# Optimization experiments

Measured on AMD Instinct MI355X. Metric: run time of the kernel, lower is better.

## Reference

```python
import jax, jax.numpy as jnp
import numpy as np

N_HEAD = 16


def _rotate_half(x):
    # interleaved split then concat, exactly as the torch module does
    x1 = x[..., ::2]
    x2 = x[..., 1::2]
    return jnp.concatenate((-x2, x1), axis=-1)


def setup_inputs() -> dict:
    key = jax.random.key(0)
    k1, k2, k3 = jax.random.split(key, 3)
    B, T, C = 4, 2048, 2048
    x = jax.random.normal(k1, (B, T, C), dtype=jnp.float32)
    w_attn = jax.random.normal(k2, (3 * C, C), dtype=jnp.float32) * 0.02
    b_attn = jnp.zeros((3 * C,), dtype=jnp.float32)
    w_proj = jax.random.normal(k3, (C, C), dtype=jnp.float32) * 0.02
    b_proj = jnp.zeros((C,), dtype=jnp.float32)
    return {"x": x, "w_attn": w_attn, "b_attn": b_attn, "w_proj": w_proj, "b_proj": b_proj}


def reference(x, w_attn, b_attn, w_proj, b_proj):
    B, T, C = x.shape
    H = N_HEAD
    D = C // H

    qkv = x @ w_attn.T + b_attn  # (B, T, 3C)
    q, k, v = jnp.split(qkv, 3, axis=2)
    # (B, H, T, D)
    q = q.reshape(B, T, H, D).transpose(0, 2, 1, 3)
    k = k.reshape(B, T, H, D).transpose(0, 2, 1, 3)
    v = v.reshape(B, T, H, D).transpose(0, 2, 1, 3)

    # RoPE tables (buffer inv_freq computed from head_dim)
    inv_freq = 1.0 / (10000.0 ** (jnp.arange(0, D, 2, dtype=jnp.float32) / D))
    t = jnp.arange(T, dtype=jnp.float32)
    freqs = t[:, None] * inv_freq[None, :]            # (T, D/2)
    emb = jnp.concatenate((freqs, freqs), axis=-1)    # (T, D)
    cos, sin = jnp.cos(emb), jnp.sin(emb)

    # module's (nonstandard) rotary application: returns q_cos + q_sin
    rq, rk = _rotate_half(q), _rotate_half(k)
    q = (q * cos - rq * sin) + (q * sin + rq * cos)
    k = (k * cos - rk * sin) + (k * sin + rk * cos)

    # causal SDPA
    scale = 1.0 / jnp.sqrt(jnp.asarray(D, dtype=x.dtype))
    scores = jnp.einsum("bhqd,bhkd->bhqk", q, k) * scale
    causal = jnp.tril(jnp.ones((T, T), dtype=bool))
    scores = jnp.where(causal, scores, jnp.asarray(-1e30, dtype=scores.dtype))
    att = jax.nn.softmax(scores, axis=-1)
    y = jnp.einsum("bhqk,bhkd->bhqd", att, v)

    y = y.transpose(0, 2, 1, 3).reshape(B, T, C)
    return y @ w_proj.T + b_proj
```

## Files before the change

### kernel.cpp

```cpp
#include <hip/hip_runtime.h>

#define T_SEQ 2048
#define DHEAD 128
#define NHEAD 16
#define CDIM  2048
#define BATCH 4

typedef __bf16 v8bf __attribute__((ext_vector_type(8)));
typedef __bf16 v4bf __attribute__((ext_vector_type(4)));
typedef __bf16 v2bf __attribute__((ext_vector_type(2)));
typedef float  v4f  __attribute__((ext_vector_type(4)));

#define MFMA16(a,b,c) __builtin_amdgcn_mfma_f32_16x16x32_bf16(a,b,c,0,0,0)
#define GLDS16(g,l) __builtin_amdgcn_global_load_lds( \
    (__attribute__((address_space(1))) void*)(g), \
    (__attribute__((address_space(3))) void*)(l), 16, 0, 0)

__global__ __launch_bounds__(256) void cvt_all(const float* __restrict__ x,
                                               const float* __restrict__ wa,
                                               const float* __restrict__ wp,
                                               __bf16* __restrict__ xo,
                                               __bf16* __restrict__ wao,
                                               __bf16* __restrict__ wpo,
                                               float2* __restrict__ rt) {
  int i = blockIdx.x * 256 + threadIdx.x;
  int stride = gridDim.x * 256;
  for (int j = i; j < 8519680; j += stride) {
    if (j < 8388608) {
      const float* src; __bf16* dst; int off;
      if (j < 4194304)      { src = x;  dst = xo;  off = j; }
      else if (j < 7340032) { src = wa; dst = wao; off = j - 4194304; }
      else                  { src = wp; dst = wpo; off = j - 7340032; }
      float4 v = *(const float4*)(src + (size_t)off * 4);
      v4bf o = {(__bf16)v.x, (__bf16)v.y, (__bf16)v.z, (__bf16)v.w};
      *(v4bf*)(dst + (size_t)off * 4) = o;
    } else {
      int e = j - 8388608;
      int tt = e >> 6, jj = e & 63;
      float invf = exp2f((float)jj * (-13.287712379549449f / 64.f));
      float ang = (float)tt * invf;
      float c = cosf(ang), s = sinf(ang);
      rt[e] = make_float2(c + s, c - s);
    }
  }
}

#define LGKM0() { asm volatile("s_waitcnt lgkmcnt(0)" ::: "memory"); \
                  __builtin_amdgcn_sched_barrier(0); }
#define BARR()  { __builtin_amdgcn_s_barrier(); __builtin_amdgcn_sched_barrier(0); }

#define RDA(mm, kk) (*(const v8bf*)(bA + (wm16 + (mm)*32 + lr) * 128 + ((((kk)*64) + lgc) ^ swl)))
#define RDB(n, kk)  (*(const v8bf*)(bB + (wn64 + (n)*16 + lr) * 128 + ((((kk)*64) + lgc) ^ swl)))
#define MF(mm,n,kk) acc[mm][n] = MFMA16(af[(mm)&1][kk], bfr[n][kk], acc[mm][n]);

#define PH_MFMA(MM0, MM1) \
  BARR(); LGKM0(); \
  __builtin_amdgcn_s_setprio(1); \
  MF(MM0,0,0) MF(MM0,1,0) MF(MM0,2,0) MF(MM0,3,0) \
  MF(MM1,0,0) MF(MM1,1,0) MF(MM1,2,0) MF(MM1,3,0) \
  MF(MM0,0,1) MF(MM0,1,1) MF(MM0,2,1) MF(MM0,3,1) \
  MF(MM1,0,1) MF(MM1,1,1) MF(MM1,2,1) MF(MM1,3,1) \
  __builtin_amdgcn_s_setprio(0); \
  BARR();

#define STAGE_H(SRC, ks, hh, LBASE) { \
  GLDS16((SRC) + (size_t)((hh)*128)      * 2048 + (size_t)(ks)*64, lds + (LBASE) + dst0); \
  GLDS16((SRC) + (size_t)((hh)*128 + 64) * 2048 + (size_t)(ks)*64, lds + (LBASE) + 4096 + dst0); }

#define TILE(CB, ks1, ks2) { \
  const char* bA = (const char*)(lds + (CB)*32768); \
  const char* bB = bA + 32768; \
  v8bf bfr[4][2], af[2][2]; \
  af[0][0]=RDA(0,0); af[0][1]=RDA(0,1); af[1][0]=RDA(1,0); af[1][1]=RDA(1,1); \
  bfr[0][0]=RDB(0,0); bfr[0][1]=RDB(0,1); bfr[1][0]=RDB(1,0); bfr[1][1]=RDB(1,1); \
  bfr[2][0]=RDB(2,0); bfr[2][1]=RDB(2,1); bfr[3][0]=RDB(3,0); bfr[3][1]=RDB(3,1); \
  STAGE_H(Asrc, ks1, 1, ((CB)^1)*32768 + 8192); \
  PH_MFMA(0, 1) \
  af[0][0]=RDA(2,0); af[0][1]=RDA(2,1); af[1][0]=RDA(3,0); af[1][1]=RDA(3,1); \
  STAGE_H(Bsrc, ks2, 0, (CB)*32768 + 16384); \
  PH_MFMA(2, 3) \
  af[0][0]=RDA(4,0); af[0][1]=RDA(4,1); af[1][0]=RDA(5,0); af[1][1]=RDA(5,1); \
  STAGE_H(Asrc, ks2, 0, (CB)*32768); \
  PH_MFMA(4, 5) \
  af[0][0]=RDA(6,0); af[0][1]=RDA(6,1); af[1][0]=RDA(7,0); af[1][1]=RDA(7,1); \
  STAGE_H(Bsrc, ks2, 1, (CB)*32768 + 24576); \
  asm volatile("s_waitcnt vmcnt(6)" ::: "memory"); \
  PH_MFMA(6, 7) \
}

__device__ __forceinline__ void gemm256_core(
    const __bf16* __restrict__ A, const __bf16* __restrict__ Bm,
    int row0, int col0, __bf16* lds, v4f (&acc)[8][4],
    int wm16, int wn64, int lr, int lg) {
  int t = threadIdx.x;
  int wid = t >> 6;
  int lgc = lg * 16;
  int swl = (lr & 7) << 4;
#pragma unroll
  for (int mm = 0; mm < 8; ++mm)
#pragma unroll
    for (int n = 0; n < 4; ++n) acc[mm][n] = (v4f){0.f, 0.f, 0.f, 0.f};

  int srow = t >> 3;
  int scol = (((t & 7) ^ ((t >> 3) & 7)) << 3);
  const __bf16* Asrc = A  + (size_t)(row0 + srow) * 2048 + scol;
  const __bf16* Bsrc = Bm + (size_t)(col0 + srow) * 2048 + scol;
  int dst0 = wid << 9;

  STAGE_H(Asrc, 0, 0, 0);
  STAGE_H(Asrc, 0, 1, 8192);
  STAGE_H(Bsrc, 0, 0, 16384);
  STAGE_H(Bsrc, 0, 1, 24576);
  STAGE_H(Bsrc, 1, 0, 32768 + 16384);
  STAGE_H(Asrc, 1, 0, 32768);
  STAGE_H(Bsrc, 1, 1, 32768 + 24576);
  asm volatile("s_waitcnt vmcnt(6)" ::: "memory");
  BARR();

  for (int m = 0; m < 32; m += 2) {
    TILE(0, m + 1, (m + 2) & 31)
    TILE(1, (m + 2) & 31, (m + 3) & 31)
  }
  asm volatile("s_waitcnt vmcnt(0)" ::: "memory");
}

__global__ __launch_bounds__(512, 2) void gemm_qkv8(
    const __bf16* __restrict__ A, const __bf16* __restrict__ Bm,
    const float* __restrict__ bias, const float2* __restrict__ rt,
    __bf16* __restrict__ Qb, __bf16* __restrict__ Kb, __bf16* __restrict__ Vt) {
  extern __shared__ __bf16 lds[];
  int t = threadIdx.x, wid = t >> 6, l = t & 63;
  int lr = l & 15, lg = l >> 4;
  int wm16 = (wid >> 2) * 16, wn64 = (wid & 3) * 64;
  int bid = blockIdx.x;
  int xcd = bid & 7, idx = bid >> 3;
  int res = idx & 31, grp = idx >> 5;
  int row0 = (xcd * 4 + (res >> 3)) * 256;
  int col0 = (grp * 8 + (res & 7)) * 256;
  v4f acc[8][4];
  gemm256_core(A, Bm, row0, col0, lds, acc, wm16, wn64, lr, lg);

  if (col0 >= 4096) {
    int h0 = (col0 & 2047) >> 7;
    int bb = row0 >> 11;
    int t0 = row0 & 2047;
    int d_r = t >> 1, half = t & 1;
    int hh = h0 + (d_r >> 7), dd = d_r & 127;
#pragma unroll
    for (int mm = 0; mm < 8; ++mm) {
      __syncthreads();
#pragma unroll
      for (int n = 0; n < 4; ++n) {
        int d_loc = wn64 + n * 16 + lr;
        float bv = bias[col0 + d_loc];
        v4bf pv = {(__bf16)(acc[mm][n][0] + bv), (__bf16)(acc[mm][n][1] + bv),
                   (__bf16)(acc[mm][n][2] + bv), (__bf16)(acc[mm][n][3] + bv)};
        *(v4bf*)&lds[d_loc * 40 + wm16 + lg * 4] = pv;
      }
      __syncthreads();
      size_t vbase = ((size_t)((bb * NHEAD + hh) * DHEAD + dd)) * T_SEQ
                   + t0 + mm * 32 + half * 16;
      v8bf x0 = *(const v8bf*)&lds[d_r * 40 + half * 16];
      v8bf x1 = *(const v8bf*)&lds[d_r * 40 + half * 16 + 8];
      *(v8bf*)&Vt[vbase] = x0;
      *(v8bf*)&Vt[vbase + 8] = x1;
    }
    return;
  }

  __syncthreads();
#pragma unroll
  for (int n = 0; n < 4; ++n) {
    int c_loc = wn64 + n * 16 + lr;
    float bv = bias[col0 + c_loc];
#pragma unroll
    for (int mm = 0; mm < 8; ++mm) {
#pragma unroll
      for (int rr = 0; rr < 4; ++rr) {
        int r_loc = wm16 + mm * 32 + lg * 4 + rr;
        *(__bf16*)((char*)lds + r_loc * 512 + ((2 * c_loc) ^ ((r_loc & 31) << 4)))
            = (__bf16)(acc[mm][n][rr] + bv);
      }
    }
  }
  __syncthreads();
  {
    int tensor = col0 >> 11;
    int h0 = (col0 & 2047) >> 7;
    int bb = row0 >> 11;
    int t0 = row0 & 2047;
    __bf16* QK = tensor ? Kb : Qb;
    int d = l;
    float sgn = (d < 32) ? -1.f : 1.f;
    int mOff = 4 * d;
    int pOff = (d < 32) ? (8 * d) : (8 * d - 256);
    int tOff = ((2 * d) & 63) * 8;
#pragma unroll 4
    for (int i = 0; i < 64; ++i) {
      int p = wid * 64 + i;
      int u = p >> 8, r = p & 255;
      int tt = t0 + r;
      const char* lrow_ = (const char*)lds + r * 512;
      int swz = (r & 31) << 4;
      int cb = u * 256;
      v2bf xm = *(const v2bf*)(lrow_ + ((cb + mOff) ^ swz));
      v4bf xp = *(const v4bf*)(lrow_ + ((cb + pOff) ^ swz));
      float4 tv = *(const float4*)((const char*)(rt + (size_t)tt * 64) + tOff);
      float p1 = (d < 32) ? (float)xp[1] : (float)xp[0];
      float p2 = (d < 32) ? (float)xp[3] : (float)xp[2];
      float o1 = (float)xm[0] * tv.x + sgn * p1 * tv.y;
      float o2 = (float)xm[1] * tv.z + sgn * p2 * tv.w;
      v2bf ov = {(__bf16)o1, (__bf16)o2};
      __bf16* dst = QK + ((size_t)(bb * NHEAD + h0 + u) * T_SEQ + tt) * DHEAD;
      *(v2bf*)(dst + 2 * d) = ov;
    }
  }
}

__global__ __launch_bounds__(512, 2) void gemm_out8(
    const __bf16* __restrict__ A, const __bf16* __restrict__ Bm,
    const float* __restrict__ bias, float* __restrict__ C) {
  extern __shared__ __bf16 lds[];
  int t = threadIdx.x, wid = t >> 6, l = t & 63;
  int lr = l & 15, lg = l >> 4;
  int wm16 = (wid >> 2) * 16, wn64 = (wid & 3) * 64;
  int bid = blockIdx.x;
  int xcd = bid & 7, idx = bid >> 3;
  int row0 = (xcd * 4 + idx / 8) * 256;
  int col0 = (idx % 8) * 256;
  v4f acc[8][4];
  gemm256_core(A, Bm, row0, col0, lds, acc, wm16, wn64, lr, lg);
#pragma unroll
  for (int n = 0; n < 4; ++n) {
    int col = col0 + wn64 + n * 16 + lr;
    float bv = bias[col];
#pragma unroll
    for (int mm = 0; mm < 8; ++mm) {
#pragma unroll
      for (int rr = 0; rr < 4; ++rr) {
        int mg = row0 + wm16 + mm * 32 + lg * 4 + rr;
        C[(size_t)mg * CDIM + col] = acc[mm][n][rr] + bv;
      }
    }
  }
}

__global__ __launch_bounds__(512, 2) void attn_fwd(
    const __bf16* __restrict__ Qb, const __bf16* __restrict__ Kb,
    const __bf16* __restrict__ Vt, __bf16* __restrict__ Y) {
  __shared__ __bf16 lK[64 * 128];
  __shared__ __bf16 lV[128 * 64];
  __shared__ __bf16 plds[8][16][72];
  int t = threadIdx.x, w = t >> 6, l = t & 63;
  int lr = l & 15, lg = l >> 4;
  int id = blockIdx.x;
  int xcd = id & 7, s = id >> 3;
  int bh = xcd * 8 + (s & 7);
  int g = s >> 3;
  int k = (g < 4) ? (7 - g) : (g - 4);
  int qb = k * 256;
  int b = bh >> 4, h = bh & 15;
  int q0 = qb + w * 32;
  const __bf16* Qh = Qb + (size_t)bh * T_SEQ * DHEAD;
  const __bf16* Kh = Kb + (size_t)bh * T_SEQ * DHEAD;
  const __bf16* Vh = Vt + (size_t)bh * DHEAD * T_SEQ;

  v8bf qf[2][4];
#pragma unroll
  for (int j = 0; j < 2; ++j)
#pragma unroll
    for (int c = 0; c < 4; ++c)
      qf[j][c] = *(const v8bf*)&Qh[(size_t)(q0 + j * 16 + lr) * DHEAD + c * 32 + lg * 8];

  v4f o[2][8];
#pragma unroll
  for (int j = 0; j < 2; ++j)
#pragma unroll
    for (int c = 0; c < 8; ++c) o[j][c] = (v4f){0.f, 0.f, 0.f, 0.f};
  float mrow[2] = {-1e30f, -1e30f}, lrow[2] = {0.f, 0.f};
  const float SCALE2 = 0.12751743f;

  int kRow = t >> 4;
  int kSrc = (((t & 15) * 16) ^ ((kRow & 7) << 4)) >> 1;
  int vRow = t >> 3;
  int vSrc = (((t & 7) * 16) ^ ((vRow & 7) << 4)) >> 1;
  __bf16* lKd0 = lK + w * 512 + l * 8;
  __bf16* lKd1 = lK + 4096 + w * 512 + l * 8;
  __bf16* lVd0 = lV + w * 512 + l * 8;
  __bf16* lVd1 = lV + 4096 + w * 512 + l * 8;

  v8bf kr0 = *(const v8bf*)&Kh[(size_t)(kRow) * DHEAD + kSrc];
  v8bf kr1 = *(const v8bf*)&Kh[(size_t)(32 + kRow) * DHEAD + kSrc];
  v8bf vr0 = *(const v8bf*)&Vh[(size_t)(vRow) * T_SEQ + vSrc];
  v8bf vr1 = *(const v8bf*)&Vh[(size_t)(64 + vRow) * T_SEQ + vSrc];

  int kvEnd = qb + 192;
  for (int kv0 = 0; kv0 <= kvEnd; kv0 += 64) {
    __syncthreads();
    *(v8bf*)lKd0 = kr0; *(v8bf*)lKd1 = kr1;
    *(v8bf*)lVd0 = vr0; *(v8bf*)lVd1 = vr1;
    __syncthreads();
    if (kv0 + 64 <= kvEnd) {
      kr0 = *(const v8bf*)&Kh[(size_t)(kv0 + 64 + kRow) * DHEAD + kSrc];
      kr1 = *(const v8bf*)&Kh[(size_t)(kv0 + 96 + kRow) * DHEAD + kSrc];
      vr0 = *(const v8bf*)&Vh[(size_t)(vRow) * T_SEQ + kv0 + 64 + vSrc];
      vr1 = *(const v8bf*)&Vh[(size_t)(64 + vRow) * T_SEQ + kv0 + 64 + vSrc];
    }

    if (kv0 <= q0 + 31) {
      v4f s2[2][4];
#pragma unroll
      for (int j = 0; j < 2; ++j)
#pragma unroll
        for (int f = 0; f < 4; ++f) s2[j][f] = (v4f){0.f, 0.f, 0.f, 0.f};
      __builtin_amdgcn_s_setprio(1);
#pragma unroll
      for (int f = 0; f < 4; ++f) {
        int row = f * 16 + lr;
        int sw = (row & 7) << 4;
#pragma unroll
        for (int c = 0; c < 4; ++c) {
          v8bf kf = *(const v8bf*)((const char*)lK + row * 256 + ((c * 64 + lg * 16) ^ sw));
          s2[0][f] = MFMA16(kf, qf[0][c], s2[0][f]);
          s2[1][f] = MFMA16(kf, qf[1][c], s2[1][f]);
        }
      }
      __builtin_amdgcn_s_setprio(0);

      v8bf pa[2][2];
#pragma unroll
      for (int j = 0; j < 2; ++j) {
        int qg = q0 + j * 16 + lr;
        bool needMask = (kv0 + 63 > q0 + j * 16);
        float p[16];
        float mt = -1e30f;
#pragma unroll
        for (int f = 0; f < 4; ++f)
#pragma unroll
          for (int r = 0; r < 4; ++r) {
            float v = s2[j][f][r] * SCALE2;
            if (needMask && (kv0 + f * 16 + lg * 4 + r > qg)) v = -1e30f;
            p[f * 4 + r] = v;
            mt = fmaxf(mt, v);
          }
        mt = fmaxf(mt, __shfl_xor(mt, 16));
        mt = fmaxf(mt, __shfl_xor(mt, 32));
        if (!__all(mt <= mrow[j] + 8.0f)) {
          float mnew = fmaxf(mrow[j], mt);
          float corr = exp2f(mrow[j] - mnew);
          mrow[j] = mnew;
          lrow[j] *= corr;
          float cf[4];
#pragma unroll
          for (int r = 0; r < 4; ++r) cf[r] = __shfl(corr, lg * 4 + r);
#pragma unroll
          for (int c = 0; c < 8; ++c)
#pragma unroll
            for (int r = 0; r < 4; ++r) o[j][c][r] *= cf[r];
        }
        float psum = 0.f;
#pragma unroll
        for (int r = 0; r < 16; ++r) { p[r] = exp2f(p[r] - mrow[j]); psum += p[r]; }
        psum += __shfl_xor(psum, 16);
        psum += __shfl_xor(psum, 32);
        lrow[j] += psum;
#pragma unroll
        for (int f = 0; f < 4; ++f) {
          v4bf pv = {(__bf16)p[f * 4], (__bf16)p[f * 4 + 1],
                     (__bf16)p[f * 4 + 2], (__bf16)p[f * 4 + 3]};
          *(v4bf*)&plds[w][lr][f * 16 + lg * 4] = pv;
        }
        asm volatile("s_waitcnt lgkmcnt(0)" ::: "memory");
        pa[j][0] = *(const v8bf*)&plds[w][lr][lg * 8];
        pa[j][1] = *(const v8bf*)&plds[w][lr][32 + lg * 8];
      }

      __builtin_amdgcn_s_setprio(1);
#pragma unroll
      for (int c = 0; c < 8; ++c) {
        int row = c * 16 + lr;
        int sw = (row & 7) << 4;
        v8bf vf0 = *(const v8bf*)((const char*)lV + row * 128 + ((lg * 16) ^ sw));
        v8bf vf1 = *(const v8bf*)((const char*)lV + row * 128 + ((64 + lg * 16) ^ sw));
        o[0][c] = MFMA16(pa[0][0], vf0, o[0][c]);
        o[0][c] = MFMA16(pa[0][1], vf1, o[0][c]);
        o[1][c] = MFMA16(pa[1][0], vf0, o[1][c]);
        o[1][c] = MFMA16(pa[1][1], vf1, o[1][c]);
      }
      __builtin_amdgcn_s_setprio(0);
    }
  }

  size_t ybase = ((size_t)b * T_SEQ) * CDIM + (size_t)h * DHEAD;
#pragma unroll
  for (int j = 0; j < 2; ++j) {
    float rf[4];
#pragma unroll
    for (int r = 0; r < 4; ++r)
      rf[r] = __builtin_amdgcn_rcpf(__shfl(lrow[j], lg * 4 + r));
#pragma unroll
    for (int c = 0; c < 8; ++c) {
#pragma unroll
      for (int r = 0; r < 4; ++r) {
        int qq = q0 + j * 16 + lg * 4 + r;
        Y[ybase + (size_t)qq * CDIM + c * 16 + lr] = (__bf16)(o[j][c][r] * rf[r]);
      }
    }
  }
}

extern "C" void kernel_launch(void* const* d_in, const int* in_sizes, int n_in,
                              void* d_out, int out_size, void* d_ws, size_t ws_size,
                              hipStream_t stream) {
  const float* x      = (const float*)d_in[0];
  const float* w_attn = (const float*)d_in[1];
  const float* b_attn = (const float*)d_in[2];
  const float* w_proj = (const float*)d_in[3];
  const float* b_proj = (const float*)d_in[4];
  float* out = (float*)d_out;

  char* ws = (char*)d_ws;
  __bf16* xbf  = (__bf16*)(ws);
  __bf16* wabf = (__bf16*)(ws + 33554432);
  __bf16* wpbf = (__bf16*)(ws + 58720256);
  __bf16* Qb   = (__bf16*)(ws + 67108864);
  __bf16* Kb   = (__bf16*)(ws + 100663296);
  __bf16* Vt   = (__bf16*)(ws + 134217728);
  float2* rtab = (float2*)(ws + 167772160);
  __bf16* Y    = xbf;

  (void)hipFuncSetAttribute((const void*)gemm_qkv8,
                            hipFuncAttributeMaxDynamicSharedMemorySize, 131072);
  (void)hipFuncSetAttribute((const void*)gemm_out8,
                            hipFuncAttributeMaxDynamicSharedMemorySize, 131072);

  cvt_all<<<2048, 256, 0, stream>>>(x, w_attn, w_proj, xbf, wabf, wpbf, rtab);

  gemm_qkv8<<<768, 512, 131072, stream>>>(xbf, wabf, b_attn, rtab, Qb, Kb, Vt);

  attn_fwd<<<512, 512, 0, stream>>>(Qb, Kb, Vt, Y);

  gemm_out8<<<256, 512, 131072, stream>>>(Y, wpbf, b_proj, out);
}
```

Measured before the change: 421.0 us.

## Stage QKV GEMM B operand through registers instead of direct global-to-LDS loads

Adds a new GEMM core for the QKV projection. The A tile is still loaded straight into LDS with global_load_lds, while the B tile is prefetched into registers one k-step ahead and written to LDS at the start of the next tile. The aim is to spread global loads across the MFMA phases and ease pressure on the direct-to-LDS path. Launch bounds drop from 2 blocks per CU to 1, which frees registers for the prefetch buffers but reduces the latency hiding that came from running two blocks per CU.

```diff
diff --git a/kernel.cpp b/kernel.cpp
--- a/kernel.cpp
+++ b/kernel.cpp
@@ -124,7 +124,87 @@
   asm volatile("s_waitcnt vmcnt(0)" ::: "memory");
 }
 
-__global__ __launch_bounds__(512, 2) void gemm_qkv8(
+#define STAGE_A2(ks, CB, HH) { \
+  GLDS16(Asrc + (size_t)((HH)*128)      * 2048 + (size_t)(ks)*64, lds + (CB)*32768 + (HH)*8192 + dst0); \
+  GLDS16(Asrc + (size_t)((HH)*128 + 64) * 2048 + (size_t)(ks)*64, lds + (CB)*32768 + (HH)*8192 + 4096 + dst0); }
+
+#define LOAD_B2A(R, ks) { \
+  R##0 = *(const v8bf*)(Bsrc + (size_t)(ks)*64); \
+  R##1 = *(const v8bf*)(Bsrc + (size_t)64*2048 + (size_t)(ks)*64); }
+#define LOAD_B2B(R, ks) { \
+  R##2 = *(const v8bf*)(Bsrc + (size_t)128*2048 + (size_t)(ks)*64); \
+  R##3 = *(const v8bf*)(Bsrc + (size_t)192*2048 + (size_t)(ks)*64); }
+
+#define WRITE_B2(R, CB) { \
+  char* dWB = (char*)lds + (CB)*65536 + 32768 + tid16; \
+  *(v8bf*)(dWB)         = R##0; \
+  *(v8bf*)(dWB +  8192) = R##1; \
+  *(v8bf*)(dWB + 16384) = R##2; \
+  *(v8bf*)(dWB + 24576) = R##3; }
+
+#define TILE_Q(CB, RW, RL, ksA, ksB) { \
+  const char* bA = (const char*)lds + (CB)*65536; \
+  const char* bB = bA + 32768; \
+  WRITE_B2(RW, (CB)^1); \
+  v8bf bfr[4][2], af[2][2]; \
+  af[0][0]=RDA(0,0); af[0][1]=RDA(0,1); af[1][0]=RDA(1,0); af[1][1]=RDA(1,1); \
+  bfr[0][0]=RDB(0,0); bfr[0][1]=RDB(0,1); bfr[1][0]=RDB(1,0); bfr[1][1]=RDB(1,1); \
+  bfr[2][0]=RDB(2,0); bfr[2][1]=RDB(2,1); bfr[3][0]=RDB(3,0); bfr[3][1]=RDB(3,1); \
+  STAGE_A2(ksA, (CB)^1, 0); \
+  PH_MFMA(0, 1) \
+  af[0][0]=RDA(2,0); af[0][1]=RDA(2,1); af[1][0]=RDA(3,0); af[1][1]=RDA(3,1); \
+  STAGE_A2(ksA, (CB)^1, 1); \
+  PH_MFMA(2, 3) \
+  af[0][0]=RDA(4,0); af[0][1]=RDA(4,1); af[1][0]=RDA(5,0); af[1][1]=RDA(5,1); \
+  __builtin_amdgcn_sched_barrier(0); \
+  LOAD_B2A(RL, ksB); \
+  PH_MFMA(4, 5) \
+  af[0][0]=RDA(6,0); af[0][1]=RDA(6,1); af[1][0]=RDA(7,0); af[1][1]=RDA(7,1); \
+  LOAD_B2B(RL, ksB); \
+  asm volatile("s_waitcnt vmcnt(4)" ::: "memory"); \
+  PH_MFMA(6, 7) \
+}
+
+__device__ __forceinline__ void gemm256q_core(
+    const __bf16* __restrict__ A, const __bf16* __restrict__ Bm,
+    int row0, int col0, __bf16* lds, v4f (&acc)[8][4],
+    int wm16, int wn64, int lr, int lg) {
+  int t = threadIdx.x;
+  int wid = t >> 6;
+  int lgc = lg * 16;
+  int swl = (lr & 7) << 4;
+  int tid16 = t * 16;
+#pragma unroll
+  for (int mm = 0; mm < 8; ++mm)
+#pragma unroll
+    for (int n = 0; n < 4; ++n) acc[mm][n] = (v4f){0.f, 0.f, 0.f, 0.f};
+
+  int srow = t >> 3;
+  int scol = (((t & 7) ^ ((t >> 3) & 7)) << 3);
+  const __bf16* Asrc = A  + (size_t)(row0 + srow) * 2048 + scol;
+  const __bf16* Bsrc = Bm + (size_t)(col0 + srow) * 2048 + scol;
+  int dst0 = wid << 9;
+
+  v8bf bx0, bx1, bx2, bx3, by0, by1, by2, by3;
+
+  LOAD_B2A(by, 0); LOAD_B2B(by, 0);
+  __builtin_amdgcn_sched_barrier(0);
+  STAGE_A2(0, 0, 0); STAGE_A2(0, 0, 1);
+  __builtin_amdgcn_sched_barrier(0);
+  WRITE_B2(by, 0);
+  LOAD_B2A(by, 1); LOAD_B2B(by, 1);
+  asm volatile("s_waitcnt vmcnt(4)" ::: "memory");
+  asm volatile("s_waitcnt lgkmcnt(0)" ::: "memory");
+  BARR();
+
+  for (int m = 0; m < 32; m += 2) {
+    TILE_Q(0, by, bx, (m + 1) & 31, (m + 2) & 31)
+    TILE_Q(1, bx, by, (m + 2) & 31, (m + 3) & 31)
+  }
+  asm volatile("s_waitcnt vmcnt(0)" ::: "memory");
+}
+
+__global__ __launch_bounds__(512, 1) void gemm_qkv8(
     const __bf16* __restrict__ A, const __bf16* __restrict__ Bm,
     const float* __restrict__ bias, const float2* __restrict__ rt,
     __bf16* __restrict__ Qb, __bf16* __restrict__ Kb, __bf16* __restrict__ Vt) {
@@ -138,7 +218,7 @@
   int row0 = (xcd * 4 + (res >> 3)) * 256;
   int col0 = (grp * 8 + (res & 7)) * 256;
   v4f acc[8][4];
-  gemm256_core(A, Bm, row0, col0, lds, acc, wm16, wn64, lr, lg);
+  gemm256q_core(A, Bm, row0, col0, lds, acc, wm16, wn64, lr, lg);
 
   if (col0 >= 4096) {
     int h0 = (col0 & 2047) >> 7;
```

Result: slower. 451.3 us (+7.2%).
